# Kernel tuning notes

Measured on AMD Instinct MI355X. Metric: run time of the kernel, lower is better.

## Reference

```python
import jax, jax.numpy as jnp
import numpy as np

N_ATOMS = 200000
N_CHANNELS = 4
N_EDGES = 12800000
PREFACTOR = 1.0


def setup_inputs() -> dict:
    key = jax.random.key(0)
    k1, k2, k3, k4, k5 = jax.random.split(key, 5)
    charges = jax.random.normal(k1, (N_ATOMS, N_CHANNELS), dtype=jnp.float32)
    cell = jax.random.normal(k2, (3, 3), dtype=jnp.float32)
    positions = jax.random.normal(k3, (N_ATOMS, 3), dtype=jnp.float32)
    neighbor_indices = jax.random.randint(k4, (N_EDGES, 2), 0, N_ATOMS, dtype=jnp.int32)
    # distances in (0.5, 5.5) to keep 1/r well-conditioned
    neighbor_distances = jax.random.uniform(k5, (N_EDGES,), dtype=jnp.float32,
                                            minval=0.5, maxval=5.5)
    return {
        "charges": charges,
        "cell": cell,
        "positions": positions,
        "neighbor_indices": neighbor_indices,
        "neighbor_distances": neighbor_distances,
    }


def reference(charges, cell, positions, neighbor_indices, neighbor_distances):
    # Potential.from_dist for a Coulomb potential with smearing=None: v(r) = 1/r
    potentials_bare = 1.0 / neighbor_distances  # [n_edges]
    atom_is = neighbor_indices[:, 0]
    atom_js = neighbor_indices[:, 1]
    # gather charge of neighbor j, weight by pair potential, scatter-add into atom i
    contributions_is = charges[atom_js] * potentials_bare[:, None]  # [n_edges, n_channels]
    potential = jnp.zeros_like(charges).at[atom_is].add(contributions_is)
    # half neighbor list (full_neighbor_list=False): symmetric term into atom j
    contributions_js = charges[atom_is] * potentials_bare[:, None]
    potential = potential.at[atom_js].add(contributions_js)
    return PREFACTOR * (potential * 0.5)  # [n_atoms, n_channels]
```

## Files before the change

### kernel.cpp

```cpp
#include <hip/hip_runtime.h>


#define BLOCK   256
#define NBLK    1024
#define NBLK_LG 10
#define AB_LOG  10
#define A_B     1024
#define MAXNB   256

static __device__ __forceinline__ unsigned long long nt_u64(const void* p) {
    return __builtin_nontemporal_load((const unsigned long long*)p);
}
static __device__ __forceinline__ float nt_f32(const float* p) {
    return __builtin_nontemporal_load(p);
}

__global__ __launch_bounds__(BLOCK) void k_hist(
    const int2* __restrict__ nbr, int* __restrict__ blk_hist,
    int n_edges, int nb)
{
    __shared__ int h[MAXNB];
    for (int i = threadIdx.x; i < nb; i += blockDim.x) h[i] = 0;
    __syncthreads();
    int per = (n_edges + gridDim.x - 1) / gridDim.x;
    int lo = blockIdx.x * per;
    int hi = min(lo + per, n_edges);
    #pragma unroll 4
    for (int e = lo + threadIdx.x; e < hi; e += blockDim.x) {
        unsigned long long v = nt_u64(&nbr[e]);
        int ix = (int)(v & 0xffffffffu);
        int iy = (int)(v >> 32);
        atomicAdd(&h[ix >> AB_LOG], 1);
        atomicAdd(&h[iy >> AB_LOG], 1);
    }
    __syncthreads();
    for (int i = threadIdx.x; i < nb; i += blockDim.x)
        blk_hist[i * NBLK + blockIdx.x] = h[i];
}

__global__ __launch_bounds__(NBLK) void k_rowscan(
    const int* __restrict__ blk_hist, int* __restrict__ offs,
    int* __restrict__ totals)
{
    __shared__ int a[NBLK];
    int b = blockIdx.x, t = threadIdx.x;
    int v = blk_hist[b * NBLK + t];
    a[t] = v;
    __syncthreads();
    for (int off = 1; off < NBLK; off <<= 1) {
        int x = (t >= off) ? a[t - off] : 0;
        __syncthreads();
        a[t] += x;
        __syncthreads();
    }
    offs[b * NBLK + t] = a[t] - v;
    if (t == NBLK - 1) totals[b] = a[t];
}

__global__ __launch_bounds__(MAXNB) void k_bases(
    const int* __restrict__ totals, int* __restrict__ bases, int nb)
{
    __shared__ int a[MAXNB];
    int t = threadIdx.x;
    int v = (t < nb) ? totals[t] : 0;
    a[t] = v;
    __syncthreads();
    for (int off = 1; off < MAXNB; off <<= 1) {
        int x = (t >= off) ? a[t - off] : 0;
        __syncthreads();
        a[t] += x;
        __syncthreads();
    }
    if (t < nb) bases[t] = a[t] - v;
}

__global__ void k_addbase(int* __restrict__ offs, const int* __restrict__ bases, int n)
{
    int i = blockIdx.x * blockDim.x + threadIdx.x;
    if (i < n) offs[i] += bases[i >> NBLK_LG];
}

__global__ __launch_bounds__(BLOCK) void k_scatter(
    const int2* __restrict__ nbr, const float* __restrict__ dist,
    const int* __restrict__ offs, uint2* __restrict__ tuples,
    int n_edges, int nb)
{
    __shared__ int cur[MAXNB];
    for (int i = threadIdx.x; i < nb; i += blockDim.x)
        cur[i] = offs[i * NBLK + blockIdx.x];
    __syncthreads();
    int per = (n_edges + gridDim.x - 1) / gridDim.x;
    int lo = blockIdx.x * per;
    int hi = min(lo + per, n_edges);
    #pragma unroll 2
    for (int e = lo + threadIdx.x; e < hi; e += blockDim.x) {
        unsigned long long v = nt_u64(&nbr[e]);
        int ix = (int)(v & 0xffffffffu);
        int iy = (int)(v >> 32);
        float w = 0.5f / nt_f32(&dist[e]);
        unsigned wb = __float_as_uint(w);
        int pi = atomicAdd(&cur[ix >> AB_LOG], 1);
        tuples[pi] = make_uint2((unsigned)(ix & (A_B - 1)) | ((unsigned)iy << AB_LOG), wb);
        int pj = atomicAdd(&cur[iy >> AB_LOG], 1);
        tuples[pj] = make_uint2((unsigned)(iy & (A_B - 1)) | ((unsigned)ix << AB_LOG), wb);
    }
}

__global__ __launch_bounds__(BLOCK) void k_accum(
    const uint2* __restrict__ tuples, const float4* __restrict__ charges,
    const int* __restrict__ bases, const int* __restrict__ totals,
    float* __restrict__ partials, int nslice)
{
    __shared__ float acc[A_B * 4];
    int b = blockIdx.x / nslice;
    int s = blockIdx.x % nslice;
    for (int i = threadIdx.x; i < A_B * 4; i += blockDim.x) acc[i] = 0.f;
    __syncthreads();
    int start = bases[b], cnt = totals[b];
    int lo = start + (int)((long long)cnt * s / nslice);
    int hi = start + (int)((long long)cnt * (s + 1) / nslice);

    int p = lo + threadIdx.x;
    for (; p + 3 * BLOCK < hi; p += 4 * BLOCK) {
        uint2 t0 = tuples[p];
        uint2 t1 = tuples[p + BLOCK];
        uint2 t2 = tuples[p + 2 * BLOCK];
        uint2 t3 = tuples[p + 3 * BLOCK];
        float4 c0 = charges[t0.x >> AB_LOG];
        float4 c1 = charges[t1.x >> AB_LOG];
        float4 c2 = charges[t2.x >> AB_LOG];
        float4 c3 = charges[t3.x >> AB_LOG];
        float w0 = __uint_as_float(t0.y), w1 = __uint_as_float(t1.y);
        float w2 = __uint_as_float(t2.y), w3 = __uint_as_float(t3.y);
        int d0 = (t0.x & (A_B - 1)) * 4, d1 = (t1.x & (A_B - 1)) * 4;
        int d2 = (t2.x & (A_B - 1)) * 4, d3 = (t3.x & (A_B - 1)) * 4;
        atomicAdd(&acc[d0 + 0], c0.x * w0); atomicAdd(&acc[d0 + 1], c0.y * w0);
        atomicAdd(&acc[d0 + 2], c0.z * w0); atomicAdd(&acc[d0 + 3], c0.w * w0);
        atomicAdd(&acc[d1 + 0], c1.x * w1); atomicAdd(&acc[d1 + 1], c1.y * w1);
        atomicAdd(&acc[d1 + 2], c1.z * w1); atomicAdd(&acc[d1 + 3], c1.w * w1);
        atomicAdd(&acc[d2 + 0], c2.x * w2); atomicAdd(&acc[d2 + 1], c2.y * w2);
        atomicAdd(&acc[d2 + 2], c2.z * w2); atomicAdd(&acc[d2 + 3], c2.w * w2);
        atomicAdd(&acc[d3 + 0], c3.x * w3); atomicAdd(&acc[d3 + 1], c3.y * w3);
        atomicAdd(&acc[d3 + 2], c3.z * w3); atomicAdd(&acc[d3 + 3], c3.w * w3);
    }
    for (; p < hi; p += BLOCK) {
        uint2 t = tuples[p];
        float4 c = charges[t.x >> AB_LOG];
        float w = __uint_as_float(t.y);
        int d = (t.x & (A_B - 1)) * 4;
        atomicAdd(&acc[d + 0], c.x * w); atomicAdd(&acc[d + 1], c.y * w);
        atomicAdd(&acc[d + 2], c.z * w); atomicAdd(&acc[d + 3], c.w * w);
    }
    __syncthreads();
    float* outp = partials + (size_t)blockIdx.x * (A_B * 4);
    for (int i = threadIdx.x; i < A_B * 4; i += blockDim.x) outp[i] = acc[i];
}

__global__ void k_final(const float4* __restrict__ partials,
                        float4* __restrict__ out, int n_atoms, int nslice)
{
    int a = blockIdx.x * blockDim.x + threadIdx.x;
    if (a >= n_atoms) return;
    int b = a >> AB_LOG;
    int local = a & (A_B - 1);
    const float4* p = partials + (size_t)(b * nslice) * A_B + local;
    float4 r = make_float4(0.f, 0.f, 0.f, 0.f);
    for (int s = 0; s < nslice; ++s) {
        float4 t = p[(size_t)s * A_B];
        r.x += t.x; r.y += t.y; r.z += t.z; r.w += t.w;
    }
    out[a] = r;
}

__global__ __launch_bounds__(BLOCK) void edge_scatter_agent(
    const float4* __restrict__ charges, const int2* __restrict__ nbr,
    const float* __restrict__ dist, float* __restrict__ out, int n_edges)
{
    int e = blockIdx.x * blockDim.x + threadIdx.x;
    if (e >= n_edges) return;
    int2 ij = nbr[e];
    float w = 0.5f / dist[e];
    float4 cj = charges[ij.y];
    float4 ci = charges[ij.x];
    float* oi = out + (size_t)ij.x * 4;
    float* oj = out + (size_t)ij.y * 4;
    atomicAdd(oi + 0, cj.x * w); atomicAdd(oi + 1, cj.y * w);
    atomicAdd(oi + 2, cj.z * w); atomicAdd(oi + 3, cj.w * w);
    atomicAdd(oj + 0, ci.x * w); atomicAdd(oj + 1, ci.y * w);
    atomicAdd(oj + 2, ci.z * w); atomicAdd(oj + 3, ci.w * w);
}

extern "C" void kernel_launch(void* const* d_in, const int* in_sizes, int n_in,
                              void* d_out, int out_size, void* d_ws, size_t ws_size,
                              hipStream_t stream)
{
    const float4* charges = (const float4*)d_in[0];
    const int2*   nbr     = (const int2*)d_in[3];
    const float*  dist    = (const float*)d_in[4];

    int n_edges = in_sizes[4];
    int n_atoms = out_size / 4;
    int nb = (n_atoms + A_B - 1) >> AB_LOG;

    size_t n_pairs = (size_t)2 * n_edges;
    char*  w   = (char*)d_ws;
    size_t off = 0;
    auto alloc = [&](size_t bytes) -> void* {
        void* p = w + off;
        off += (bytes + 255) & ~(size_t)255;
        return p;
    };
    uint2* tuples   = (uint2*)alloc(n_pairs * sizeof(uint2));
    int*   blk_hist = (int*)  alloc((size_t)nb * NBLK * sizeof(int));
    int*   offs     = (int*)  alloc((size_t)nb * NBLK * sizeof(int));
    int*   totals   = (int*)  alloc((size_t)nb * sizeof(int));
    int*   bases    = (int*)  alloc((size_t)nb * sizeof(int));

    size_t slice_bytes = (size_t)nb * A_B * 4 * sizeof(float);
    int nslice = 16;
    while (nslice > 1 && off + (size_t)nslice * slice_bytes > ws_size) nslice >>= 1;
    float* partials = (float*)alloc((size_t)nslice * slice_bytes);

    if (off <= ws_size && nb <= MAXNB) {
        k_hist   <<<NBLK, BLOCK, 0, stream>>>(nbr, blk_hist, n_edges, nb);
        k_rowscan<<<nb,   NBLK,  0, stream>>>(blk_hist, offs, totals);
        k_bases  <<<1,    MAXNB, 0, stream>>>(totals, bases, nb);
        k_addbase<<<(nb * NBLK + 255) / 256, 256, 0, stream>>>(offs, bases, nb * NBLK);
        k_scatter<<<NBLK, BLOCK, 0, stream>>>(nbr, dist, offs, tuples, n_edges, nb);
        k_accum  <<<nb * nslice, BLOCK, 0, stream>>>(tuples, charges, bases, totals,
                                                     partials, nslice);
        k_final  <<<(n_atoms + 255) / 256, 256, 0, stream>>>(
            (const float4*)partials, (float4*)d_out, n_atoms, nslice);
    } else {
        hipMemsetAsync(d_out, 0, (size_t)out_size * sizeof(float), stream);
        edge_scatter_agent<<<(n_edges + BLOCK - 1) / BLOCK, BLOCK, 0, stream>>>(
            charges, nbr, dist, (float*)d_out, n_edges);
    }
}
```

Baseline: 1.030 ms.

## Privatize histogram per wave, planarize accum LDS layout, prefetch tuples

The histogram kernel now gives each wavefront its own shared-memory histogram, which cuts atomic contention, and sums the four copies at the end. The accumulation kernel switches the shared accumulator from interleaved atom×channel to channel-planar layout to reduce LDS bank conflicts on atomics. It also software-pipelines tuple loads with non-temporal prefetch of the next group, and writes partials with non-temporal stores. The scatter unroll goes from 2 to 4, and k_final reads the planar partials layout, which gives up its float4 loads.

```diff
diff --git a/kernel.cpp b/kernel.cpp
--- a/kernel.cpp
+++ b/kernel.cpp
@@ -14,14 +14,18 @@
 static __device__ __forceinline__ float nt_f32(const float* p) {
     return __builtin_nontemporal_load(p);
 }
+static __device__ __forceinline__ void nt_store(float* p, float v) {
+    __builtin_nontemporal_store(v, p);
+}
 
 __global__ __launch_bounds__(BLOCK) void k_hist(
     const int2* __restrict__ nbr, int* __restrict__ blk_hist,
     int n_edges, int nb)
 {
-    __shared__ int h[MAXNB];
-    for (int i = threadIdx.x; i < nb; i += blockDim.x) h[i] = 0;
-    __syncthreads();
+    __shared__ int h[4 * MAXNB];
+    for (int i = threadIdx.x; i < 4 * MAXNB; i += blockDim.x) h[i] = 0;
+    __syncthreads();
+    int* hw = h + (threadIdx.x >> 6) * MAXNB;
     int per = (n_edges + gridDim.x - 1) / gridDim.x;
     int lo = blockIdx.x * per;
     int hi = min(lo + per, n_edges);
@@ -30,12 +34,13 @@
         unsigned long long v = nt_u64(&nbr[e]);
         int ix = (int)(v & 0xffffffffu);
         int iy = (int)(v >> 32);
-        atomicAdd(&h[ix >> AB_LOG], 1);
-        atomicAdd(&h[iy >> AB_LOG], 1);
+        atomicAdd(&hw[ix >> AB_LOG], 1);
+        atomicAdd(&hw[iy >> AB_LOG], 1);
     }
     __syncthreads();
     for (int i = threadIdx.x; i < nb; i += blockDim.x)
-        blk_hist[i * NBLK + blockIdx.x] = h[i];
+        blk_hist[i * NBLK + blockIdx.x] =
+            h[i] + h[MAXNB + i] + h[2 * MAXNB + i] + h[3 * MAXNB + i];
 }
 
 __global__ __launch_bounds__(NBLK) void k_rowscan(
@@ -92,7 +97,7 @@
     int per = (n_edges + gridDim.x - 1) / gridDim.x;
     int lo = blockIdx.x * per;
     int hi = min(lo + per, n_edges);
-    #pragma unroll 2
+    #pragma unroll 4
     for (int e = lo + threadIdx.x; e < hi; e += blockDim.x) {
         unsigned long long v = nt_u64(&nbr[e]);
         int ix = (int)(v & 0xffffffffu);
@@ -111,65 +116,100 @@
     const int* __restrict__ bases, const int* __restrict__ totals,
     float* __restrict__ partials, int nslice)
 {
-    __shared__ float acc[A_B * 4];
+    __shared__ float acc[4 * A_B];
     int b = blockIdx.x / nslice;
     int s = blockIdx.x % nslice;
-    for (int i = threadIdx.x; i < A_B * 4; i += blockDim.x) acc[i] = 0.f;
+    for (int i = threadIdx.x; i < 4 * A_B; i += blockDim.x) acc[i] = 0.f;
     __syncthreads();
     int start = bases[b], cnt = totals[b];
     int lo = start + (int)((long long)cnt * s / nslice);
     int hi = start + (int)((long long)cnt * (s + 1) / nslice);
 
+    const unsigned long long* tp = (const unsigned long long*)tuples;
+
     int p = lo + threadIdx.x;
-    for (; p + 3 * BLOCK < hi; p += 4 * BLOCK) {
-        uint2 t0 = tuples[p];
-        uint2 t1 = tuples[p + BLOCK];
-        uint2 t2 = tuples[p + 2 * BLOCK];
-        uint2 t3 = tuples[p + 3 * BLOCK];
-        float4 c0 = charges[t0.x >> AB_LOG];
-        float4 c1 = charges[t1.x >> AB_LOG];
-        float4 c2 = charges[t2.x >> AB_LOG];
-        float4 c3 = charges[t3.x >> AB_LOG];
-        float w0 = __uint_as_float(t0.y), w1 = __uint_as_float(t1.y);
-        float w2 = __uint_as_float(t2.y), w3 = __uint_as_float(t3.y);
-        int d0 = (t0.x & (A_B - 1)) * 4, d1 = (t1.x & (A_B - 1)) * 4;
-        int d2 = (t2.x & (A_B - 1)) * 4, d3 = (t3.x & (A_B - 1)) * 4;
-        atomicAdd(&acc[d0 + 0], c0.x * w0); atomicAdd(&acc[d0 + 1], c0.y * w0);
-        atomicAdd(&acc[d0 + 2], c0.z * w0); atomicAdd(&acc[d0 + 3], c0.w * w0);
-        atomicAdd(&acc[d1 + 0], c1.x * w1); atomicAdd(&acc[d1 + 1], c1.y * w1);
-        atomicAdd(&acc[d1 + 2], c1.z * w1); atomicAdd(&acc[d1 + 3], c1.w * w1);
-        atomicAdd(&acc[d2 + 0], c2.x * w2); atomicAdd(&acc[d2 + 1], c2.y * w2);
-        atomicAdd(&acc[d2 + 2], c2.z * w2); atomicAdd(&acc[d2 + 3], c2.w * w2);
-        atomicAdd(&acc[d3 + 0], c3.x * w3); atomicAdd(&acc[d3 + 1], c3.y * w3);
-        atomicAdd(&acc[d3 + 2], c3.z * w3); atomicAdd(&acc[d3 + 3], c3.w * w3);
+    unsigned long long t0 = 0, t1 = 0, t2 = 0, t3 = 0;
+    bool have = (p + 3 * BLOCK < hi);
+    if (have) {
+        t0 = nt_u64(&tp[p]);
+        t1 = nt_u64(&tp[p + BLOCK]);
+        t2 = nt_u64(&tp[p + 2 * BLOCK]);
+        t3 = nt_u64(&tp[p + 3 * BLOCK]);
+    }
+    while (have) {
+        int np = p + 4 * BLOCK;
+        bool nhave = (np + 3 * BLOCK < hi);
+        unsigned u0 = (unsigned)t0, u1 = (unsigned)t1;
+        unsigned u2 = (unsigned)t2, u3 = (unsigned)t3;
+        float4 c0 = charges[u0 >> AB_LOG];
+        float4 c1 = charges[u1 >> AB_LOG];
+        float4 c2 = charges[u2 >> AB_LOG];
+        float4 c3 = charges[u3 >> AB_LOG];
+        float w0 = __uint_as_float((unsigned)(t0 >> 32));
+        float w1 = __uint_as_float((unsigned)(t1 >> 32));
+        float w2 = __uint_as_float((unsigned)(t2 >> 32));
+        float w3 = __uint_as_float((unsigned)(t3 >> 32));
+        int d0 = u0 & (A_B - 1), d1 = u1 & (A_B - 1);
+        int d2 = u2 & (A_B - 1), d3 = u3 & (A_B - 1);
+        if (nhave) {
+            t0 = nt_u64(&tp[np]);
+            t1 = nt_u64(&tp[np + BLOCK]);
+            t2 = nt_u64(&tp[np + 2 * BLOCK]);
+            t3 = nt_u64(&tp[np + 3 * BLOCK]);
+        }
+        atomicAdd(&acc[d0], c0.x * w0);
+        atomicAdd(&acc[A_B + d0], c0.y * w0);
+        atomicAdd(&acc[2 * A_B + d0], c0.z * w0);
+        atomicAdd(&acc[3 * A_B + d0], c0.w * w0);
+        atomicAdd(&acc[d1], c1.x * w1);
+        atomicAdd(&acc[A_B + d1], c1.y * w1);
+        atomicAdd(&acc[2 * A_B + d1], c1.z * w1);
+        atomicAdd(&acc[3 * A_B + d1], c1.w * w1);
+        atomicAdd(&acc[d2], c2.x * w2);
+        atomicAdd(&acc[A_B + d2], c2.y * w2);
+        atomicAdd(&acc[2 * A_B + d2], c2.z * w2);
+        atomicAdd(&acc[3 * A_B + d2], c2.w * w2);
+        atomicAdd(&acc[d3], c3.x * w3);
+        atomicAdd(&acc[A_B + d3], c3.y * w3);
+        atomicAdd(&acc[2 * A_B + d3], c3.z * w3);
+        atomicAdd(&acc[3 * A_B + d3], c3.w * w3);
+        p = np;
+        have = nhave;
     }
     for (; p < hi; p += BLOCK) {
-        uint2 t = tuples[p];
-        float4 c = charges[t.x >> AB_LOG];
-        float w = __uint_as_float(t.y);
-        int d = (t.x & (A_B - 1)) * 4;
-        atomicAdd(&acc[d + 0], c.x * w); atomicAdd(&acc[d + 1], c.y * w);
-        atomicAdd(&acc[d + 2], c.z * w); atomicAdd(&acc[d + 3], c.w * w);
-    }
-    __syncthreads();
-    float* outp = partials + (size_t)blockIdx.x * (A_B * 4);
-    for (int i = threadIdx.x; i < A_B * 4; i += blockDim.x) outp[i] = acc[i];
-}
-
-__global__ void k_final(const float4* __restrict__ partials,
+        unsigned long long t = nt_u64(&tp[p]);
+        unsigned u = (unsigned)t;
+        float4 c = charges[u >> AB_LOG];
+        float w = __uint_as_float((unsigned)(t >> 32));
+        int d = u & (A_B - 1);
+        atomicAdd(&acc[d], c.x * w);
+        atomicAdd(&acc[A_B + d], c.y * w);
+        atomicAdd(&acc[2 * A_B + d], c.z * w);
+        atomicAdd(&acc[3 * A_B + d], c.w * w);
+    }
+    __syncthreads();
+    float* outp = partials + (size_t)blockIdx.x * (4 * A_B);
+    for (int i = threadIdx.x; i < 4 * A_B; i += blockDim.x)
+        nt_store(&outp[i], acc[i]);
+}
+
+__global__ void k_final(const float* __restrict__ partials,
                         float4* __restrict__ out, int n_atoms, int nslice)
 {
     int a = blockIdx.x * blockDim.x + threadIdx.x;
     if (a >= n_atoms) return;
     int b = a >> AB_LOG;
     int local = a & (A_B - 1);
-    const float4* p = partials + (size_t)(b * nslice) * A_B + local;
-    float4 r = make_float4(0.f, 0.f, 0.f, 0.f);
+    const float* base = partials + (size_t)(b * nslice) * (4 * A_B) + local;
+    float r0 = 0.f, r1 = 0.f, r2 = 0.f, r3 = 0.f;
     for (int s = 0; s < nslice; ++s) {
-        float4 t = p[(size_t)s * A_B];
-        r.x += t.x; r.y += t.y; r.z += t.z; r.w += t.w;
-    }
-    out[a] = r;
+        const float* p = base + (size_t)s * (4 * A_B);
+        r0 += p[0];
+        r1 += p[A_B];
+        r2 += p[2 * A_B];
+        r3 += p[3 * A_B];
+    }
+    out[a] = make_float4(r0, r1, r2, r3);
 }
 
 __global__ __launch_bounds__(BLOCK) void edge_scatter_agent(
@@ -230,7 +270,7 @@
         k_accum  <<<nb * nslice, BLOCK, 0, stream>>>(tuples, charges, bases, totals,
                                                      partials, nslice);
         k_final  <<<(n_atoms + 255) / 256, 256, 0, stream>>>(
-            (const float4*)partials, (float4*)d_out, n_atoms, nslice);
+            partials, (float4*)d_out, n_atoms, nslice);
     } else {
         hipMemsetAsync(d_out, 0, (size_t)out_size * sizeof(float), stream);
         edge_scatter_agent<<<(n_edges + BLOCK - 1) / BLOCK, BLOCK, 0, stream>>>(
```

After: 1.034 ms. About the same (+0.4%).
